# Kernel tuning notes

Hardware: AMD Instinct MI355X
Metric: run time of the kernel (lower is better)

The kernel has to match this reference:

```python
import jax, jax.numpy as jnp
import numpy as np

C, H, W = 3, 224, 224
P = 14  # patches per row
PS = H // P  # 16
PATCH_DIM = C * PS * PS  # 768
HIDDEN = 768


def patchify(images):
    # images: [n, c, h, w] -> [n, P*P, c*PS*PS], flatten order (c, ph, pw)
    n = images.shape[0]
    x = images.reshape(n, C, P, PS, P, PS)
    x = x.transpose(0, 2, 4, 1, 3, 5)  # [n, Pi, Pj, c, ps, ps]
    return x.reshape(n, P * P, PATCH_DIM)


def setup_inputs() -> dict:
    key = jax.random.key(0)
    k1, k2, k3 = jax.random.split(key, 3)
    images = jax.random.normal(k1, (128, C, H, W), dtype=jnp.float32)
    # nn.Linear(patch_embedding_dim, hidden_dim): weight [out, in], bias [out]
    bound = 1.0 / np.sqrt(PATCH_DIM)
    W_lin = jax.random.uniform(k2, (HIDDEN, PATCH_DIM), minval=-bound, maxval=bound, dtype=jnp.float32)
    b_lin = jax.random.uniform(k3, (HIDDEN,), minval=-bound, maxval=bound, dtype=jnp.float32)
    cls_token = jnp.ones((1, HIDDEN), dtype=jnp.float32)
    return {"images": images, "W_lin": W_lin, "b_lin": b_lin, "cls_token": cls_token}


def reference(images, W_lin, b_lin, cls_token):
    patches = patchify(images)                        # [n, 196, 768]
    hidden = jnp.einsum('npd,hd->nph', patches, W_lin) + b_lin  # [n, 196, H]
    n = images.shape[0]
    cls = jnp.broadcast_to(cls_token[None], (n, 1, HIDDEN))
    return jnp.concatenate([cls, hidden], axis=1)     # [n, 197, H]
```

## Files before the change

kernel.cpp:

```cpp
#include <hip/hip_runtime.h>
#include <cstdint>


#define PGRID 14
#define PSZ   16
#define CHN   3
#define IMGW  224
#define KDIM  768
#define NDIM  768
#define NPATCH 196

typedef short bf16x8 __attribute__((ext_vector_type(8)));
typedef short short8v __attribute__((ext_vector_type(8)));
typedef float f32x4  __attribute__((ext_vector_type(4)));

__device__ __forceinline__ short bf16rne(float f) {
    uint32_t u = __builtin_bit_cast(uint32_t, f);
    u += 0x7FFFu + ((u >> 16) & 1u);
    return (short)(u >> 16);
}

__device__ __forceinline__ short8v cvt8(float4 v0, float4 v1) {
    short8v s;
    s[0] = bf16rne(v0.x); s[1] = bf16rne(v0.y); s[2] = bf16rne(v0.z); s[3] = bf16rne(v0.w);
    s[4] = bf16rne(v1.x); s[5] = bf16rne(v1.y); s[6] = bf16rne(v1.z); s[7] = bf16rne(v1.w);
    return s;
}

__global__ __launch_bounds__(256) void prep_all(
    const float* __restrict__ img, const float* __restrict__ Wl,
    const float* __restrict__ cls, short* __restrict__ A,
    short* __restrict__ Wb, float* __restrict__ out, int n_img)
{
    const int IMG8 = n_img * (CHN * IMGW * IMGW / 8);
    const int W8   = KDIM * NDIM / 8;
    int t = blockIdx.x * 256 + threadIdx.x;

    if (t < IMG8) {
        int w8    = t % (IMGW / 8);
        int rest  = t / (IMGW / 8);
        int h     = rest % IMGW;
        int rest2 = rest / IMGW;
        int c     = rest2 % CHN;
        int im    = rest2 / CHN;

        float4 v0 = *(const float4*)(img + (long)t * 8);
        float4 v1 = *(const float4*)(img + (long)t * 8 + 4);

        int Pi = h >> 4;
        int ph = h & 15;
        int Pj = w8 >> 1;
        int pw = (w8 & 1) * 8;
        int m  = im * NPATCH + Pi * PGRID + Pj;
        int k  = (c << 8) + (ph << 4) + pw;
        *(short8v*)(A + (long)m * KDIM + k) = cvt8(v0, v1);
    } else if (t < IMG8 + W8) {
        int u = t - IMG8;
        float4 v0 = *(const float4*)(Wl + (long)u * 8);
        float4 v1 = *(const float4*)(Wl + (long)u * 8 + 4);
        *(short8v*)(Wb + (long)u * 8) = cvt8(v0, v1);
    } else {
        int u = t - IMG8 - W8;
        if (u < n_img * (NDIM / 8)) {
            int im = u / (NDIM / 8);
            int k8 = u - im * (NDIM / 8);
            float4 v0 = *(const float4*)(cls + k8 * 8);
            float4 v1 = *(const float4*)(cls + k8 * 8 + 4);
            float* dst = out + (long)im * 197 * NDIM + k8 * 8;
            *(float4*)dst = v0;
            *(float4*)(dst + 4) = v1;
        }
    }
}

__global__ __launch_bounds__(256) void vit_gemm3(
    const short* __restrict__ A, const short* __restrict__ B,
    const float* __restrict__ bias, float* __restrict__ out,
    int M, int mgroups)
{
    const int bid = blockIdx.x;
    const int xcd = bid & 7;
    const int s   = bid >> 3;
    const int gq  = s / 6;
    const int j   = s - gq * 6;
    const int g   = gq * 8 + xcd;
    if (g >= mgroups) return;
    const int m0 = g * 128;
    const int n0 = j * 128;

    __shared__ short As[128 * 64];
    __shared__ short Bs[128 * 64];

    const int tid = threadIdx.x;
    const int wave = tid >> 6;
    const int lane = tid & 63;

    const int srow = tid >> 3;
    const int sk   = (tid & 7) ^ (srow & 7);
    const long abase = (long)(m0 + srow) * KDIM + sk * 8;
    const long bbase = (long)(n0 + srow) * KDIM + sk * 8;

    const int wm = (wave & 1) * 64;
    const int wn = (wave >> 1) * 64;
    const int wq = lane >> 4;
    const int lr = lane & 15;
    const int blk0 = ((wq)     ^ (lr & 7)) * 8;
    const int blk1 = ((wq + 4) ^ (lr & 7)) * 8;

    f32x4 acc[4][4] = {};
    bf16x8 ra[4], rb[4];

    #pragma unroll
    for (int jj = 0; jj < 4; ++jj) {
        ra[jj] = *(const bf16x8*)(A + abase + (long)jj * 32 * KDIM);
        rb[jj] = *(const bf16x8*)(B + bbase + (long)jj * 32 * KDIM);
    }

    for (int kk = 0; kk < KDIM; kk += 64) {
        #pragma unroll
        for (int jj = 0; jj < 4; ++jj) {
            *(bf16x8*)(&As[(jj * 256 + tid) * 8]) = ra[jj];
            *(bf16x8*)(&Bs[(jj * 256 + tid) * 8]) = rb[jj];
        }
        __syncthreads();

        if (kk + 64 < KDIM) {
            #pragma unroll
            for (int jj = 0; jj < 4; ++jj) {
                ra[jj] = *(const bf16x8*)(A + abase + (long)jj * 32 * KDIM + kk + 64);
                rb[jj] = *(const bf16x8*)(B + bbase + (long)jj * 32 * KDIM + kk + 64);
            }
        }

        #pragma unroll
        for (int ks = 0; ks < 2; ++ks) {
            const int blk = ks ? blk1 : blk0;
            bf16x8 a[4], b[4];
            #pragma unroll
            for (int i = 0; i < 4; ++i)
                a[i] = *(const bf16x8*)(&As[(wm + i * 16 + lr) * 64 + blk]);
            #pragma unroll
            for (int i = 0; i < 4; ++i)
                b[i] = *(const bf16x8*)(&Bs[(wn + i * 16 + lr) * 64 + blk]);
            #pragma unroll
            for (int i = 0; i < 4; ++i)
                #pragma unroll
                for (int jm = 0; jm < 4; ++jm)
                    acc[i][jm] = __builtin_amdgcn_mfma_f32_16x16x32_bf16(a[i], b[jm], acc[i][jm], 0, 0, 0);
        }
        __syncthreads();
    }

    float bv[4];
    #pragma unroll
    for (int jm = 0; jm < 4; ++jm) bv[jm] = bias[n0 + wn + jm * 16 + lr];

    #pragma unroll
    for (int i = 0; i < 4; ++i) {
        #pragma unroll
        for (int r = 0; r < 4; ++r) {
            int gm = m0 + wm + i * 16 + wq * 4 + r;
            if (gm < M) {
                int im = gm / NPATCH;
                int p  = gm - im * NPATCH;
                long orow = ((long)im * 197 + 1 + p) * (long)NDIM;
                #pragma unroll
                for (int jm = 0; jm < 4; ++jm)
                    out[orow + n0 + wn + jm * 16 + lr] = acc[i][jm][r] + bv[jm];
            }
        }
    }
}

#define LDSTR 40
__global__ __launch_bounds__(256) void vit_gemm_fb(
    const float* __restrict__ img, const float* __restrict__ Wl,
    const float* __restrict__ bias, float* __restrict__ out, int n_img)
{
    const int M = n_img * NPATCH;
    __shared__ short As[128 * LDSTR];
    __shared__ short Bs[128 * LDSTR];
    const int tid = threadIdx.x;
    const int m0 = blockIdx.y * 128;
    const int n0 = blockIdx.x * 128;
    const int col4  = tid & 7;
    const int rbase = tid >> 3;
    long arow[4];
    for (int rr = 0; rr < 4; ++rr) {
        int m = m0 + rbase + rr * 32;
        int mm = (m < M) ? m : (M - 1);
        int im = mm / NPATCH;
        int p  = mm % NPATCH;
        int Pi = p / PGRID;
        int Pj = p % PGRID;
        arow[rr] = ((long)(im * CHN) * IMGW + Pi * PSZ) * IMGW + Pj * PSZ;
    }
    const int lane = tid & 63;
    const int wave = tid >> 6;
    const int wm = (wave & 1) * 64;
    const int wn = (wave >> 1) * 64;
    const int wq = lane >> 4;
    const int lr = lane & 15;
    f32x4 acc[4][4] = {};
    for (int k0 = 0; k0 < KDIM; k0 += 32) {
        {
            int k  = k0 + col4 * 4;
            int c  = k >> 8;
            int ph = (k >> 4) & 15;
            int pw = k & 15;
            long koff = (long)(c * IMGW + ph) * IMGW + pw;
            #pragma unroll
            for (int rr = 0; rr < 4; ++rr) {
                const float4 v = *(const float4*)(img + arow[rr] + koff);
                int row = rbase + rr * 32;
                short4 s;
                s.x = bf16rne(v.x); s.y = bf16rne(v.y);
                s.z = bf16rne(v.z); s.w = bf16rne(v.w);
                *(short4*)(&As[row * LDSTR + col4 * 4]) = s;
            }
        }
        {
            int k = k0 + col4 * 4;
            #pragma unroll
            for (int rr = 0; rr < 4; ++rr) {
                int nrow = rbase + rr * 32;
                const float4 v = *(const float4*)(Wl + (long)(n0 + nrow) * KDIM + k);
                short4 s;
                s.x = bf16rne(v.x); s.y = bf16rne(v.y);
                s.z = bf16rne(v.z); s.w = bf16rne(v.w);
                *(short4*)(&Bs[nrow * LDSTR + col4 * 4]) = s;
            }
        }
        __syncthreads();
        bf16x8 a[4], b[4];
        #pragma unroll
        for (int i = 0; i < 4; ++i)
            a[i] = *(const bf16x8*)(&As[(wm + i * 16 + lr) * LDSTR + wq * 8]);
        #pragma unroll
        for (int i = 0; i < 4; ++i)
            b[i] = *(const bf16x8*)(&Bs[(wn + i * 16 + lr) * LDSTR + wq * 8]);
        #pragma unroll
        for (int i = 0; i < 4; ++i)
            #pragma unroll
            for (int j = 0; j < 4; ++j)
                acc[i][j] = __builtin_amdgcn_mfma_f32_16x16x32_bf16(a[i], b[j], acc[i][j], 0, 0, 0);
        __syncthreads();
    }
    float bv[4];
    #pragma unroll
    for (int j = 0; j < 4; ++j) bv[j] = bias[n0 + wn + j * 16 + lr];
    #pragma unroll
    for (int i = 0; i < 4; ++i) {
        #pragma unroll
        for (int r = 0; r < 4; ++r) {
            int gm = m0 + wm + i * 16 + wq * 4 + r;
            if (gm < M) {
                int im = gm / NPATCH;
                int p  = gm % NPATCH;
                long orow = ((long)im * 197 + 1 + p) * (long)NDIM;
                #pragma unroll
                for (int j = 0; j < 4; ++j)
                    out[orow + n0 + wn + j * 16 + lr] = acc[i][j][r] + bv[j];
            }
        }
    }
}

__global__ __launch_bounds__(256) void cls_fill(
    const float* __restrict__ cls, float* __restrict__ out, int n_img)
{
    int i = blockIdx.x * 256 + threadIdx.x;
    if (i < n_img * NDIM) {
        int im = i / NDIM;
        int n  = i - im * NDIM;
        out[(long)im * 197 * NDIM + n] = cls[n];
    }
}

extern "C" void kernel_launch(void* const* d_in, const int* in_sizes, int n_in,
                              void* d_out, int out_size, void* d_ws, size_t ws_size,
                              hipStream_t stream) {
    const float* img  = (const float*)d_in[0];
    const float* Wl   = (const float*)d_in[1];
    const float* bias = (const float*)d_in[2];
    const float* cls  = (const float*)d_in[3];
    float* out = (float*)d_out;

    int n_img = in_sizes[0] / (CHN * IMGW * IMGW);
    int M = n_img * NPATCH;
    int mgroups = (M + 127) / 128;
    long Mpad = (long)mgroups * 128;

    size_t need = (size_t)(Mpad * KDIM + (long)KDIM * NDIM) * sizeof(short);
    if (ws_size >= need) {
        short* A_ws = (short*)d_ws;
        short* Wb   = A_ws + Mpad * KDIM;

        int total8 = n_img * (CHN * IMGW * IMGW / 8)
                   + KDIM * NDIM / 8
                   + n_img * (NDIM / 8);
        prep_all<<<(total8 + 255) / 256, 256, 0, stream>>>(img, Wl, cls, A_ws, Wb, out, n_img);

        int gpad = (mgroups + 7) & ~7;
        int nblocks = gpad * 6;
        vit_gemm3<<<nblocks, 256, 0, stream>>>(A_ws, Wb, bias, out, M, mgroups);
    } else {
        dim3 grid(NDIM / 128, mgroups);
        vit_gemm_fb<<<grid, 256, 0, stream>>>(img, Wl, bias, out, n_img);
        int cls_elems = n_img * NDIM;
        cls_fill<<<(cls_elems + 255) / 256, 256, 0, stream>>>(cls, out, n_img);
    }
}
```

Baseline: 179.1 us.

## Double-buffer LDS tiles with two register stages in GEMM main loop

Replaces the single LDS buffer with ping-pong buffers and two register staging sets, fully unrolling the K loop by two. The next tile is written to the alternate LDS buffer while the current one feeds the MFMAs. This drops one barrier per K step and lets global loads run further ahead. In exchange LDS use doubles to 64 KB per block and the extra staging registers raise VGPR pressure, both of which can cut occupancy.

```diff
diff --git a/kernel.cpp b/kernel.cpp
--- a/kernel.cpp
+++ b/kernel.cpp
@@ -88,8 +88,10 @@
     const int m0 = g * 128;
     const int n0 = j * 128;
 
-    __shared__ short As[128 * 64];
-    __shared__ short Bs[128 * 64];
+    __shared__ short As0[128 * 64];
+    __shared__ short Bs0[128 * 64];
+    __shared__ short As1[128 * 64];
+    __shared__ short Bs1[128 * 64];
 
     const int tid = threadIdx.x;
     const int wave = tid >> 6;
@@ -108,48 +110,68 @@
     const int blk1 = ((wq + 4) ^ (lr & 7)) * 8;
 
     f32x4 acc[4][4] = {};
-    bf16x8 ra[4], rb[4];
-
-    #pragma unroll
-    for (int jj = 0; jj < 4; ++jj) {
-        ra[jj] = *(const bf16x8*)(A + abase + (long)jj * 32 * KDIM);
-        rb[jj] = *(const bf16x8*)(B + bbase + (long)jj * 32 * KDIM);
-    }
-
-    for (int kk = 0; kk < KDIM; kk += 64) {
-        #pragma unroll
-        for (int jj = 0; jj < 4; ++jj) {
-            *(bf16x8*)(&As[(jj * 256 + tid) * 8]) = ra[jj];
-            *(bf16x8*)(&Bs[(jj * 256 + tid) * 8]) = rb[jj];
-        }
+    bf16x8 sa0[4], sb0[4], sa1[4], sb1[4];
+
+#define LOADT(SA, SB, KOFF)                                                  \
+    {                                                                        \
+        _Pragma("unroll")                                                    \
+        for (int jj = 0; jj < 4; ++jj) {                                     \
+            SA[jj] = *(const bf16x8*)(A + abase + (long)jj * 32 * KDIM + (KOFF)); \
+            SB[jj] = *(const bf16x8*)(B + bbase + (long)jj * 32 * KDIM + (KOFF)); \
+        }                                                                    \
+    }
+
+#define WRITET(AS, BS, SA, SB)                                               \
+    {                                                                        \
+        _Pragma("unroll")                                                    \
+        for (int jj = 0; jj < 4; ++jj) {                                     \
+            *(bf16x8*)(&AS[(jj * 256 + tid) * 8]) = SA[jj];                  \
+            *(bf16x8*)(&BS[(jj * 256 + tid) * 8]) = SB[jj];                  \
+        }                                                                    \
+    }
+
+#define COMPUTE(AS, BS)                                                      \
+    {                                                                        \
+        _Pragma("unroll")                                                    \
+        for (int ks = 0; ks < 2; ++ks) {                                     \
+            const int blk = ks ? blk1 : blk0;                                \
+            bf16x8 a[4], b[4];                                               \
+            _Pragma("unroll")                                                \
+            for (int i = 0; i < 4; ++i)                                      \
+                a[i] = *(const bf16x8*)(&AS[(wm + i * 16 + lr) * 64 + blk]); \
+            _Pragma("unroll")                                                \
+            for (int i = 0; i < 4; ++i)                                      \
+                b[i] = *(const bf16x8*)(&BS[(wn + i * 16 + lr) * 64 + blk]); \
+            _Pragma("unroll")                                                \
+            for (int i = 0; i < 4; ++i)                                      \
+                _Pragma("unroll")                                            \
+                for (int jm = 0; jm < 4; ++jm)                               \
+                    acc[i][jm] = __builtin_amdgcn_mfma_f32_16x16x32_bf16(    \
+                        a[i], b[jm], acc[i][jm], 0, 0, 0);                   \
+        }                                                                    \
+    }
+
+    LOADT(sa0, sb0, 0)
+    LOADT(sa1, sb1, 64)
+    WRITET(As0, Bs0, sa0, sb0)
+    __syncthreads();
+
+    #pragma unroll
+    for (int u = 0; u < 6; ++u) {
+        const int t = 2 * u;
+        if (t + 1 < 12) WRITET(As1, Bs1, sa1, sb1)
+        if (t + 2 < 12) LOADT(sa0, sb0, (t + 2) * 64)
+        COMPUTE(As0, Bs0)
         __syncthreads();
-
-        if (kk + 64 < KDIM) {
-            #pragma unroll
-            for (int jj = 0; jj < 4; ++jj) {
-                ra[jj] = *(const bf16x8*)(A + abase + (long)jj * 32 * KDIM + kk + 64);
-                rb[jj] = *(const bf16x8*)(B + bbase + (long)jj * 32 * KDIM + kk + 64);
-            }
-        }
-
-        #pragma unroll
-        for (int ks = 0; ks < 2; ++ks) {
-            const int blk = ks ? blk1 : blk0;
-            bf16x8 a[4], b[4];
-            #pragma unroll
-            for (int i = 0; i < 4; ++i)
-                a[i] = *(const bf16x8*)(&As[(wm + i * 16 + lr) * 64 + blk]);
-            #pragma unroll
-            for (int i = 0; i < 4; ++i)
-                b[i] = *(const bf16x8*)(&Bs[(wn + i * 16 + lr) * 64 + blk]);
-            #pragma unroll
-            for (int i = 0; i < 4; ++i)
-                #pragma unroll
-                for (int jm = 0; jm < 4; ++jm)
-                    acc[i][jm] = __builtin_amdgcn_mfma_f32_16x16x32_bf16(a[i], b[jm], acc[i][jm], 0, 0, 0);
-        }
+        if (t + 2 < 12) WRITET(As0, Bs0, sa0, sb0)
+        if (t + 3 < 12) LOADT(sa1, sb1, (t + 3) * 64)
+        COMPUTE(As1, Bs1)
         __syncthreads();
     }
+
+#undef LOADT
+#undef WRITET
+#undef COMPUTE
 
     float bv[4];
     #pragma unroll
```

Result: faster. 174.8 us (-2.4%).
